# Optimization experiments

Hardware: AMD Instinct MI355X
Metric: run time of the kernel (lower is better)

Reference implementation:

```python
import jax, jax.numpy as jnp
import numpy as np

N_NODES = 100000
N_EDGES = 640000
D = 128
BN_EPS = 1e-5


def setup_inputs() -> dict:
    key = jax.random.key(0)
    ks = jax.random.split(key, 8)
    scale = 1.0 / np.sqrt(D)
    x = jax.random.normal(ks[0], (N_NODES, D), jnp.float32)
    edge_index = jax.random.randint(ks[1], (2, N_EDGES), 0, N_NODES, jnp.int32)
    edge_attr = jax.random.normal(ks[2], (N_EDGES,), jnp.float32)
    # SAGEConv params: lin_l applied to aggregated neighbors (has bias), lin_r to root
    W_l = jax.random.normal(ks[3], (D, D), jnp.float32) * scale
    b_l = jnp.zeros((D,), jnp.float32)
    W_r = jax.random.normal(ks[4], (D, D), jnp.float32) * scale
    # BatchNorm1d affine params
    gamma = jnp.ones((D,), jnp.float32)
    beta = jnp.zeros((D,), jnp.float32)
    return {"x": x, "edge_attr": edge_attr, "W_l": W_l, "b_l": b_l,
            "W_r": W_r, "gamma": gamma, "beta": beta, "edge_index": edge_index}


def reference(x, edge_attr, W_l, b_l, W_r, gamma, beta, edge_index):
    n = x.shape[0]
    h = jax.nn.relu(x)                               # ReLU before conv
    src, dst = edge_index[0], edge_index[1]
    msg = h[src]                                     # gather [E, D]
    agg = jax.ops.segment_sum(msg, dst, num_segments=n)          # scatter-add [N, D]
    cnt = jax.ops.segment_sum(jnp.ones((msg.shape[0], 1), h.dtype), dst,
                              num_segments=n)
    mean_agg = agg / jnp.maximum(cnt, 1.0)           # mean aggregation (clamp deg>=1)
    out = mean_agg @ W_l.T + b_l + h @ W_r.T         # SAGEConv: neighbor + root terms
    # BatchNorm1d (training mode: batch stats, biased variance)
    mu = jnp.mean(out, axis=0)
    var = jnp.mean(jnp.square(out - mu), axis=0)
    xhat = (out - mu) * jax.lax.rsqrt(var + BN_EPS)
    return xhat * gamma + beta
```

## Files before the change

kernel.cpp:

```cpp
#include <hip/hip_runtime.h>
#include <stdint.h>

#define NN 100000
#define NE 640000
#define DD 128
#define BN_EPS 1e-5f
#define NB 391
#define NROWPAD 100096
#define NTILE 782
#define GGRID 512

#define SETUP_PREPX_BLOCKS 6256
#define SETUP_PREPW_BLOCKS 128
#define SETUP_HIST_BLOCKS  2500

typedef __attribute__((ext_vector_type(8)))  short bf16x8;
typedef __attribute__((ext_vector_type(4)))  float f32x4;

static __device__ __forceinline__ float bf2f(unsigned short s) {
  return __uint_as_float(((unsigned)s) << 16);
}
static __device__ __forceinline__ unsigned short f2bf(float f) {
  unsigned u = __float_as_uint(f);
  u += 0x7FFFu + ((u >> 16) & 1u);
  return (unsigned short)(u >> 16);
}

__global__ __launch_bounds__(1024) void k_zero(int* __restrict__ deg)
{
  int i = blockIdx.x * 1024 + threadIdx.x;
  if (i < NROWPAD) deg[i] = 0;
}

__global__ __launch_bounds__(256) void k_setup(
    const float* __restrict__ x,
    const float* __restrict__ Wl, const float* __restrict__ Wr,
    const int* __restrict__ ei,
    unsigned short* __restrict__ abuf, unsigned short* __restrict__ wbf,
    int* __restrict__ deg)
{
  int b = blockIdx.x;
  if (b < SETUP_PREPX_BLOCKS) {
    int i = b * 256 + threadIdx.x;
    int row = i >> 4, cj = i & 15;
    if (row < NN) {
      const float* xp = x + (long)row * DD + cj * 8;
      float tmp[8];
      *(float4*)(tmp)     = *(const float4*)(xp);
      *(float4*)(tmp + 4) = *(const float4*)(xp + 4);
      bf16x8 o;
#pragma unroll
      for (int e = 0; e < 8; ++e) o[e] = (short)f2bf(fmaxf(tmp[e], 0.f));
      *(bf16x8*)(abuf + (long)row * 256 + DD + cj * 8) = o;
    } else {
      bf16x8 z = {};
      *(bf16x8*)(abuf + (long)row * 256 + cj * 8) = z;
      *(bf16x8*)(abuf + (long)row * 256 + DD + cj * 8) = z;
    }
  } else if (b < SETUP_PREPX_BLOCKS + SETUP_PREPW_BLOCKS) {
    int i = (b - SETUP_PREPX_BLOCKS) * 256 + threadIdx.x;
    int col = i >> 8, k = i & 255;
    float v = (k < DD) ? Wl[col * DD + k] : Wr[col * DD + (k - DD)];
    wbf[i] = f2bf(v);
  } else {
    int e = (b - SETUP_PREPX_BLOCKS - SETUP_PREPW_BLOCKS) * 256 + threadIdx.x;
    if (e < NE) atomicAdd(deg + ei[NE + e], 1);
  }
}

__global__ __launch_bounds__(256) void k_scan1(const int* __restrict__ deg,
                                               int* __restrict__ bsum)
{
  __shared__ int sc[256];
  int t = threadIdx.x;
  sc[t] = deg[blockIdx.x * 256 + t];
  __syncthreads();
  for (int s = 128; s > 0; s >>= 1) {
    if (t < s) sc[t] += sc[t + s];
    __syncthreads();
  }
  if (t == 0) bsum[blockIdx.x] = sc[0];
}

__global__ __launch_bounds__(512) void k_scan2(const int* __restrict__ bsum,
                                               int* __restrict__ boff)
{
  __shared__ int sc[512];
  int t = threadIdx.x;
  int v = (t < NB) ? bsum[t] : 0;
  sc[t] = v;
  __syncthreads();
  for (int s = 1; s < 512; s <<= 1) {
    int add = (t >= s) ? sc[t - s] : 0;
    __syncthreads();
    sc[t] += add;
    __syncthreads();
  }
  if (t < NB) boff[t] = sc[t] - v;
}

__global__ __launch_bounds__(256) void k_scan3(int* __restrict__ deg,
                                               const int* __restrict__ boff,
                                               int* __restrict__ offs)
{
  __shared__ int sc[256];
  int t = threadIdx.x;
  int i = blockIdx.x * 256 + t;
  int v = deg[i];
  sc[t] = v;
  __syncthreads();
  for (int s = 1; s < 256; s <<= 1) {
    int add = (t >= s) ? sc[t - s] : 0;
    __syncthreads();
    sc[t] += add;
    __syncthreads();
  }
  int excl = sc[t] - v + boff[blockIdx.x];
  offs[i] = excl;
  deg[i]  = excl;
}

__global__ __launch_bounds__(256) void k_fill(const int* __restrict__ ei,
                                              int* __restrict__ cursor,
                                              int* __restrict__ esrc)
{
  int e = blockIdx.x * 256 + threadIdx.x;
  if (e >= NE) return;
  int pos = atomicAdd(cursor + ei[NE + e], 1);
  esrc[pos] = ei[e];
}

__global__ __launch_bounds__(256) void k_agg(const int* __restrict__ offs,
                                             const int* __restrict__ esrc,
                                             unsigned short* __restrict__ abuf)
{
  int dst = blockIdx.x * 4 + (threadIdx.x >> 6);
  if (dst >= NN) return;
  int lane = threadIdx.x & 63;
  int q  = lane >> 4;
  int fl = lane & 15;
  int off = offs[dst], end = offs[dst + 1];
  int deg = end - off;
  float acc[8];
#pragma unroll
  for (int e = 0; e < 8; ++e) acc[e] = 0.f;

  for (int base = off; base < end; base += 64) {
    int m = end - base; if (m > 64) m = 64;
    int mysrc = (base + lane < end) ? esrc[base + lane] : NN;
    int iters = (m + 3) >> 2;
#pragma unroll 2
    for (int i = 0; i < iters; ++i) {
      int src = __shfl(mysrc, i * 4 + q);
      bf16x8 w = *(const bf16x8*)(abuf + (long)src * 256 + DD + fl * 8);
#pragma unroll
      for (int e = 0; e < 8; ++e) acc[e] += bf2f((unsigned short)w[e]);
    }
  }

#pragma unroll
  for (int e = 0; e < 8; ++e) {
    acc[e] += __shfl_xor(acc[e], 16);
    acc[e] += __shfl_xor(acc[e], 32);
  }
  if (q == 0) {
    float rinv = (deg > 0) ? 1.0f / (float)deg : 0.f;
    bf16x8 o;
#pragma unroll
    for (int e = 0; e < 8; ++e) o[e] = (short)f2bf(acc[e] * rinv);
    *(bf16x8*)(abuf + (long)dst * 256 + fl * 8) = o;
  }
}

#define GEMM_STAGE_B() \
  _Pragma("unroll") \
  for (int j = 0; j < 8; ++j) { \
    int id = j * 512 + t, col = id >> 5, seg = id & 31; \
    uint4 v = *(const uint4*)(wbf + col * 256 + seg * 8); \
    int byte = (col << 9) + (seg << 4); byte ^= (col & 7) << 4; \
    *(uint4*)((char*)blds + byte) = v; \
  } \
  __syncthreads();

#define GEMM_TILE_COMPUTE(rb) \
  { const unsigned short* ap = abuf + (long)((rb) + c15) * 256 + kg * 8; \
    _Pragma("unroll 4") \
    for (int ks = 0; ks < 8; ++ks) { \
      bf16x8 a = *(const bf16x8*)(ap + ks * 32); \
      _Pragma("unroll") \
      for (int ct = 0; ct < 8; ++ct) { \
        int byte = ((ct * 16 + c15) << 9) + (ks << 6) + (kg << 4); \
        byte ^= (c15 & 7) << 4; \
        bf16x8 b = *(const bf16x8*)((const char*)blds + byte); \
        acc[ct] = __builtin_amdgcn_mfma_f32_16x16x32_bf16(a, b, acc[ct], 0, 0, 0); \
      } \
    } }

__global__ __launch_bounds__(512, 2) void k_gemm1(
    const unsigned short* __restrict__ abuf,
    const unsigned short* __restrict__ wbf,
    float* __restrict__ partials)
{
  __shared__ __align__(16) unsigned short blds[32768];
  const int t = threadIdx.x;
  const int lane = t & 63, wv = t >> 6;
  const int c15 = lane & 15, kg = lane >> 4;

  GEMM_STAGE_B();

  float sS[8], sQ[8];
#pragma unroll
  for (int ct = 0; ct < 8; ++ct) { sS[ct] = 0.f; sQ[ct] = 0.f; }

  for (int tile = blockIdx.x; tile < NTILE; tile += GGRID) {
    int rb = tile * 128 + wv * 16;
    f32x4 acc[8];
#pragma unroll
    for (int ct = 0; ct < 8; ++ct) acc[ct] = (f32x4){0.f, 0.f, 0.f, 0.f};
    GEMM_TILE_COMPUTE(rb);
#pragma unroll
    for (int ct = 0; ct < 8; ++ct) {
#pragma unroll
      for (int r = 0; r < 4; ++r) {
        float v = acc[ct][r];
        sS[ct] += v;
        sQ[ct] += v * v;
      }
    }
  }

  __syncthreads();
  float* slds = (float*)blds;
#pragma unroll
  for (int ct = 0; ct < 8; ++ct) {
    float s = sS[ct], q = sQ[ct];
    s += __shfl_xor(s, 16); q += __shfl_xor(q, 16);
    s += __shfl_xor(s, 32); q += __shfl_xor(q, 32);
    if (lane < 16) {
      slds[wv * 256 + ct * 16 + lane] = s;
      slds[wv * 256 + 128 + ct * 16 + lane] = q;
    }
  }
  __syncthreads();
  if (t < 256) {
    float a = 0.f;
#pragma unroll
    for (int w = 0; w < 8; ++w) a += slds[w * 256 + t];
    partials[blockIdx.x * 256 + t] = a;
  }
}

__global__ __launch_bounds__(1024) void k_stats(
    const float* __restrict__ partials, const float* __restrict__ bl,
    const float* __restrict__ gamma, const float* __restrict__ beta,
    float* __restrict__ ss)
{
  __shared__ float red[4][256];
  int t = threadIdx.x & 255, g = threadIdx.x >> 8;
  float a = 0.f;
#pragma unroll 8
  for (int blk = g; blk < GGRID; blk += 4) a += partials[blk * 256 + t];
  red[g][t] = a;
  __syncthreads();
  if (threadIdx.x < 256)
    red[0][t] = red[0][t] + red[1][t] + red[2][t] + red[3][t];
  __syncthreads();
  if (threadIdx.x < 128) {
    float Sr = red[0][t], Qr = red[0][128 + t];
    float b  = bl[t];
    float S  = Sr + (float)NN * b;
    float Q  = Qr + 2.f * b * Sr + (float)NN * b * b;
    float mu  = S / (float)NN;
    float var = Q / (float)NN - mu * mu;
    float rsig = rsqrtf(var + BN_EPS);
    float sc  = gamma[t] * rsig;
    float sh2 = beta[t] - mu * sc;
    ss[t]       = sc;
    ss[128 + t] = b * sc + sh2;
  }
}

__global__ __launch_bounds__(512, 2) void k_gemm2(
    const unsigned short* __restrict__ abuf,
    const unsigned short* __restrict__ wbf,
    const float* __restrict__ ss,
    float* __restrict__ out)
{
  __shared__ __align__(16) unsigned short blds[32768];
  const int t = threadIdx.x;
  const int lane = t & 63, wv = t >> 6;
  const int c15 = lane & 15, kg = lane >> 4;

  GEMM_STAGE_B();

  float sc[8], sh2[8];
#pragma unroll
  for (int ct = 0; ct < 8; ++ct) {
    sc[ct]  = ss[ct * 16 + c15];
    sh2[ct] = ss[128 + ct * 16 + c15];
  }

  for (int tile = blockIdx.x; tile < NTILE; tile += GGRID) {
    int rb = tile * 128 + wv * 16;
    f32x4 acc[8];
#pragma unroll
    for (int ct = 0; ct < 8; ++ct) acc[ct] = (f32x4){0.f, 0.f, 0.f, 0.f};
    GEMM_TILE_COMPUTE(rb);
    if (rb + 16 <= NN) {
#pragma unroll
      for (int ct = 0; ct < 8; ++ct) {
        int col = ct * 16 + c15;
#pragma unroll
        for (int r = 0; r < 4; ++r) {
          long row = rb + kg * 4 + r;
          out[row * DD + col] = fmaf(acc[ct][r], sc[ct], sh2[ct]);
        }
      }
    } else {
#pragma unroll
      for (int ct = 0; ct < 8; ++ct) {
        int col = ct * 16 + c15;
#pragma unroll
        for (int r = 0; r < 4; ++r) {
          long row = rb + kg * 4 + r;
          if (row < NN)
            out[row * DD + col] = fmaf(acc[ct][r], sc[ct], sh2[ct]);
        }
      }
    }
  }
}

extern "C" void kernel_launch(void* const* d_in, const int* in_sizes, int n_in,
                              void* d_out, int out_size, void* d_ws, size_t ws_size,
                              hipStream_t stream)
{
  const float* x     = (const float*)d_in[0];
  const float* Wl    = (const float*)d_in[2];
  const float* bl    = (const float*)d_in[3];
  const float* Wr    = (const float*)d_in[4];
  const float* gamma = (const float*)d_in[5];
  const float* beta  = (const float*)d_in[6];
  const int*   ei    = (const int*)d_in[7];
  float* out = (float*)d_out;

  char* ws = (char*)d_ws;
  unsigned short* abuf = (unsigned short*)(ws);
  int*   esrc  = (int*)(ws + 51249152);
  int*   deg   = (int*)(ws + 53809152);
  int*   offs  = (int*)(ws + 54209536);
  int*   bsum  = (int*)(ws + 54609920);
  int*   boff  = (int*)(ws + 54611968);
  unsigned short* wbf = (unsigned short*)(ws + 54614016);
  float* partials = (float*)esrc;
  float* ssbuf    = (float*)deg;
  (void)ws_size; (void)in_sizes; (void)n_in; (void)out_size;

  k_zero  <<<98,   1024, 0, stream>>>(deg);
  k_setup <<<SETUP_PREPX_BLOCKS + SETUP_PREPW_BLOCKS + SETUP_HIST_BLOCKS,
             256, 0, stream>>>(x, Wl, Wr, ei, abuf, wbf, deg);
  k_scan1 <<<NB,    256, 0, stream>>>(deg, bsum);
  k_scan2 <<<1,     512, 0, stream>>>(bsum, boff);
  k_scan3 <<<NB,    256, 0, stream>>>(deg, boff, offs);
  k_fill  <<<2500,  256, 0, stream>>>(ei, deg, esrc);
  k_agg   <<<25000, 256, 0, stream>>>(offs, esrc, abuf);
  k_gemm1 <<<GGRID, 512, 0, stream>>>(abuf, wbf, partials);
  k_stats <<<1,    1024, 0, stream>>>(partials, bl, gamma, beta, ssbuf);
  k_gemm2 <<<GGRID, 512, 0, stream>>>(abuf, wbf, ssbuf, out);
}
```

Measured before the change: 161.8 us.

## Store the pre-norm GEMM result in bf16 and normalize in a streaming kernel

The first GEMM pass now writes its bf16-rounded output in place over the first half of each activation row. The second full GEMM pass is replaced by a lightweight elementwise kernel that reads those values and applies the batch-norm scale and shift. This removes the duplicate matrix multiply and the second load of the weights into shared memory. In exchange it adds scattered 2-byte stores in the first GEMM, a separate launch, and rounds the pre-norm result to bf16 before normalization, which costs accuracy.

```diff
diff --git a/kernel.cpp b/kernel.cpp
--- a/kernel.cpp
+++ b/kernel.cpp
@@ -197,7 +197,7 @@
     } }
 
 __global__ __launch_bounds__(512, 2) void k_gemm1(
-    const unsigned short* __restrict__ abuf,
+    unsigned short* __restrict__ abuf,
     const unsigned short* __restrict__ wbf,
     float* __restrict__ partials)
 {
@@ -220,11 +220,13 @@
     GEMM_TILE_COMPUTE(rb);
 #pragma unroll
     for (int ct = 0; ct < 8; ++ct) {
+      int col = ct * 16 + c15;
 #pragma unroll
       for (int r = 0; r < 4; ++r) {
         float v = acc[ct][r];
         sS[ct] += v;
         sQ[ct] += v * v;
+        abuf[(long)(rb + kg * 4 + r) * 256 + col] = f2bf(v);
       }
     }
   }
@@ -280,55 +282,33 @@
   }
 }
 
-__global__ __launch_bounds__(512, 2) void k_gemm2(
+__global__ __launch_bounds__(256) void k_norm(
     const unsigned short* __restrict__ abuf,
-    const unsigned short* __restrict__ wbf,
     const float* __restrict__ ss,
     float* __restrict__ out)
 {
-  __shared__ __align__(16) unsigned short blds[32768];
-  const int t = threadIdx.x;
-  const int lane = t & 63, wv = t >> 6;
-  const int c15 = lane & 15, kg = lane >> 4;
-
-  GEMM_STAGE_B();
-
-  float sc[8], sh2[8];
-#pragma unroll
-  for (int ct = 0; ct < 8; ++ct) {
-    sc[ct]  = ss[ct * 16 + c15];
-    sh2[ct] = ss[128 + ct * 16 + c15];
-  }
-
-  for (int tile = blockIdx.x; tile < NTILE; tile += GGRID) {
-    int rb = tile * 128 + wv * 16;
-    f32x4 acc[8];
-#pragma unroll
-    for (int ct = 0; ct < 8; ++ct) acc[ct] = (f32x4){0.f, 0.f, 0.f, 0.f};
-    GEMM_TILE_COMPUTE(rb);
-    if (rb + 16 <= NN) {
-#pragma unroll
-      for (int ct = 0; ct < 8; ++ct) {
-        int col = ct * 16 + c15;
-#pragma unroll
-        for (int r = 0; r < 4; ++r) {
-          long row = rb + kg * 4 + r;
-          out[row * DD + col] = fmaf(acc[ct][r], sc[ct], sh2[ct]);
-        }
-      }
-    } else {
-#pragma unroll
-      for (int ct = 0; ct < 8; ++ct) {
-        int col = ct * 16 + c15;
-#pragma unroll
-        for (int r = 0; r < 4; ++r) {
-          long row = rb + kg * 4 + r;
-          if (row < NN)
-            out[row * DD + col] = fmaf(acc[ct][r], sc[ct], sh2[ct]);
-        }
-      }
-    }
-  }
+  __shared__ float sc[128], sh[128];
+  if (threadIdx.x < 128) {
+    sc[threadIdx.x] = ss[threadIdx.x];
+    sh[threadIdx.x] = ss[128 + threadIdx.x];
+  }
+  __syncthreads();
+  int i = blockIdx.x * 256 + threadIdx.x;
+  int row = i >> 4, cj = i & 15;
+  if (row >= NN) return;
+  bf16x8 v = *(const bf16x8*)(abuf + (long)row * 256 + cj * 8);
+  int c0 = cj * 8;
+  float4 o0, o1;
+  o0.x = fmaf(bf2f((unsigned short)v[0]), sc[c0 + 0], sh[c0 + 0]);
+  o0.y = fmaf(bf2f((unsigned short)v[1]), sc[c0 + 1], sh[c0 + 1]);
+  o0.z = fmaf(bf2f((unsigned short)v[2]), sc[c0 + 2], sh[c0 + 2]);
+  o0.w = fmaf(bf2f((unsigned short)v[3]), sc[c0 + 3], sh[c0 + 3]);
+  o1.x = fmaf(bf2f((unsigned short)v[4]), sc[c0 + 4], sh[c0 + 4]);
+  o1.y = fmaf(bf2f((unsigned short)v[5]), sc[c0 + 5], sh[c0 + 5]);
+  o1.z = fmaf(bf2f((unsigned short)v[6]), sc[c0 + 6], sh[c0 + 6]);
+  o1.w = fmaf(bf2f((unsigned short)v[7]), sc[c0 + 7], sh[c0 + 7]);
+  *(float4*)(out + (long)row * DD + c0)     = o0;
+  *(float4*)(out + (long)row * DD + c0 + 4) = o1;
 }
 
 extern "C" void kernel_launch(void* const* d_in, const int* in_sizes, int n_in,
@@ -366,5 +346,5 @@
   k_agg   <<<25000, 256, 0, stream>>>(offs, esrc, abuf);
   k_gemm1 <<<GGRID, 512, 0, stream>>>(abuf, wbf, partials);
   k_stats <<<1,    1024, 0, stream>>>(partials, bl, gamma, beta, ssbuf);
-  k_gemm2 <<<GGRID, 512, 0, stream>>>(abuf, wbf, ssbuf, out);
-}
+  k_norm  <<<6250,  256, 0, stream>>>(abuf, ssbuf, out);
+}
```

Measured after the change: 162.1 us. No clear change (+0.2%).
